# Optimization experiments

Measured on AMD Instinct MI355X. Metric: run time of the kernel, lower is better.

Reference implementation:

```python
import jax, jax.numpy as jnp
import numpy as np

IN, H, HC, HQ, OUT = 7, 64, 32, 16, 3  # input, shared hidden, cell hidden, head hidden, per-task out
B, S = 256, 2048


def setup_inputs() -> dict:
    key = jax.random.key(0)
    ks = iter(jax.random.split(key, 40))
    def p(shape, scale=0.1):
        return jax.random.normal(next(ks), shape, dtype=jnp.float32) * scale
    d = {}
    d['x'] = jax.random.normal(next(ks), (B, S, IN), dtype=jnp.float32)
    # shared LSTM (torch gate order i,f,g,o)
    d['W_ih_s'] = p((4 * H, IN)); d['W_hh_s'] = p((4 * H, H))
    d['b_ih_s'] = p((4 * H,));    d['b_hh_s'] = p((4 * H,))
    # attitude cell: input = [shared_h(64), x(7)]
    d['W_ih_a'] = p((4 * HC, H + IN)); d['W_hh_a'] = p((4 * HC, HC))
    d['b_ih_a'] = p((4 * HC,));        d['b_hh_a'] = p((4 * HC,))
    # velocity cell: input = [shared_h(64), delta_att(3), x(7)]
    d['W_ih_v'] = p((4 * HC, H + OUT + IN)); d['W_hh_v'] = p((4 * HC, HC))
    d['b_ih_v'] = p((4 * HC,));              d['b_hh_v'] = p((4 * HC,))
    # position cell: input = [shared_h(64), delta_vel(3)]
    d['W_ih_p'] = p((4 * HC, H + OUT)); d['W_hh_p'] = p((4 * HC, HC))
    d['b_ih_p'] = p((4 * HC,));         d['b_hh_p'] = p((4 * HC,))
    # per-task readout MLPs (dropout is identity in eval mode)
    d['Wa1'] = p((HQ, HC)); d['ba1'] = p((HQ,)); d['Wa2'] = p((OUT, HQ)); d['ba2'] = p((OUT,))
    d['Wv1'] = p((HQ, HC)); d['bv1'] = p((HQ,)); d['Wv2'] = p((OUT, HQ)); d['bv2'] = p((OUT,))
    d['Wp1'] = p((HQ, HC)); d['bp1'] = p((HQ,)); d['Wp2'] = p((OUT, HQ)); d['bp2'] = p((OUT,))
    return d


def lstm_cell(x, h, c, Wih, Whh, bih, bhh):
    z = x @ Wih.T + h @ Whh.T + bih + bhh
    i, f, g, o = jnp.split(z, 4, axis=-1)
    c = jax.nn.sigmoid(f) * c + jax.nn.sigmoid(i) * jnp.tanh(g)
    h = jax.nn.sigmoid(o) * jnp.tanh(c)
    return h, c


def mlp(h, W1, b1, W2, b2):
    return jax.nn.relu(h @ W1.T + b1) @ W2.T + b2


def reference(x, W_ih_s, W_hh_s, b_ih_s, b_hh_s,
              W_ih_a, W_hh_a, b_ih_a, b_hh_a,
              W_ih_v, W_hh_v, b_ih_v, b_hh_v,
              W_ih_p, W_hh_p, b_ih_p, b_hh_p,
              Wa1, ba1, Wa2, ba2, Wv1, bv1, Wv2, bv2, Wp1, bp1, Wp2, bp2):
    b = x.shape[0]
    z = lambda n: jnp.zeros((b, n), x.dtype)
    carry0 = (z(H), z(H), z(HC), z(HC), z(HC), z(HC), z(HC), z(HC))

    def step(carry, xt):
        hs, cs, ha, ca, hv, cv, hp, cp = carry
        hs, cs = lstm_cell(xt, hs, cs, W_ih_s, W_hh_s, b_ih_s, b_hh_s)
        ha, ca = lstm_cell(jnp.concatenate([hs, xt], -1), ha, ca,
                           W_ih_a, W_hh_a, b_ih_a, b_hh_a)
        d_att = mlp(ha, Wa1, ba1, Wa2, ba2)
        hv, cv = lstm_cell(jnp.concatenate([hs, jax.lax.stop_gradient(d_att), xt], -1),
                           hv, cv, W_ih_v, W_hh_v, b_ih_v, b_hh_v)
        d_vel = mlp(hv, Wv1, bv1, Wv2, bv2)
        hp, cp = lstm_cell(jnp.concatenate([hs, jax.lax.stop_gradient(d_vel)], -1),
                           hp, cp, W_ih_p, W_hh_p, b_ih_p, b_hh_p)
        d_pos = mlp(hp, Wp1, bp1, Wp2, bp2)
        out = jnp.concatenate([d_att, d_vel, d_pos], -1)  # [B, 9]
        return (hs, cs, ha, ca, hv, cv, hp, cp), out

    _, ys = jax.lax.scan(step, carry0, jnp.swapaxes(x, 0, 1))  # [S, B, 9]
    return jnp.swapaxes(ys, 0, 1)  # [B, S, 9]
```

## Files before the change

kernel.cpp:

```cpp
#include <hip/hip_runtime.h>

typedef unsigned int u32;

#define NIN 7
#define NB 256
#define NS 2048

__device__ __forceinline__ float fastrcp(float x){ return __builtin_amdgcn_rcpf(x); }
__device__ __forceinline__ float sigf(float x){ return fastrcp(1.f + __expf(-x)); }
__device__ __forceinline__ float tanhf_(float x){ return 1.f - 2.f*fastrcp(1.f + __expf(2.f*x)); }

__device__ __forceinline__ u32 pkh(float a, float b){
  unsigned short ua = __builtin_bit_cast(unsigned short, (_Float16)a);
  unsigned short ub = __builtin_bit_cast(unsigned short, (_Float16)b);
  return (u32)ua | ((u32)ub << 16);
}

template<int J>
__device__ __forceinline__ float rlf(float v){
  return __uint_as_float((unsigned)__builtin_amdgcn_readlane((int)__float_as_uint(v), J));
}
__device__ __forceinline__ float rlfv(float v, int j){
  return __uint_as_float((unsigned)__builtin_amdgcn_readlane((int)__float_as_uint(v), j));
}

__device__ __forceinline__ float mxl(float acc, u32 wp, float a){
  asm("v_fma_mix_f32 %0, %1, %2, %3 op_sel_hi:[1,0,0]"
      : "=v"(acc) : "v"(wp), "s"(a), "0"(acc));
  return acc;
}
__device__ __forceinline__ float mxh(float acc, u32 wp, float a){
  asm("v_fma_mix_f32 %0, %1, %2, %3 op_sel:[1,0,0] op_sel_hi:[1,0,0]"
      : "=v"(acc) : "v"(wp), "s"(a), "0"(acc));
  return acc;
}
__device__ __forceinline__ float mxlv(float acc, u32 wp, float a){
  asm("v_fma_mix_f32 %0, %1, %2, %3 op_sel_hi:[1,0,0]"
      : "=v"(acc) : "v"(wp), "v"(a), "0"(acc));
  return acc;
}
__device__ __forceinline__ float mxhv(float acc, u32 wp, float a){
  asm("v_fma_mix_f32 %0, %1, %2, %3 op_sel:[1,0,0] op_sel_hi:[1,0,0]"
      : "=v"(acc) : "v"(wp), "v"(a), "0"(acc));
  return acc;
}

__device__ __forceinline__ float gate4(float zi, float zf, float zg, float zo, float& c){
  c = sigf(zf)*c + sigf(zi)*tanhf_(zg);
  return sigf(zo)*tanhf_(c);
}

#define XD(a0, a1, KB, v0, v1) { \
  a0 = mxlv(a0, w[(KB)+0], (v0).x); a1 = mxhv(a1, w[(KB)+0], (v0).y); \
  a0 = mxlv(a0, w[(KB)+1], (v0).z); a1 = mxhv(a1, w[(KB)+1], (v0).w); \
  a0 = mxlv(a0, w[(KB)+2], (v1).x); a1 = mxhv(a1, w[(KB)+2], (v1).y); \
  a0 = mxlv(a0, w[(KB)+3], (v1).z); a1 = mxhv(a1, w[(KB)+3], (v1).w); }

#define MX2(a0, a1, s0, s1, KA, KS, SRC) { _Pragma("unroll") \
  for (int k_ = 0; k_ < 32; k_++){ \
    float e0_ = rlfv(SRC, 2*k_), e1_ = rlfv(SRC, 2*k_+1); \
    a0 = mxl(a0, w[(KA)+k_], e0_); a1 = mxh(a1, w[(KA)+k_], e1_); \
    s0 = mxl(s0, w[(KS)+k_], e0_); s1 = mxh(s1, w[(KS)+k_], e1_); } }

#define MX1(a0, a1, KA, SRC) { _Pragma("unroll") \
  for (int k_ = 0; k_ < 32; k_++){ \
    float e0_ = rlfv(SRC, 2*k_), e1_ = rlfv(SRC, 2*k_+1); \
    a0 = mxl(a0, w[(KA)+k_], e0_); a1 = mxh(a1, w[(KA)+k_], e1_); } }

#define MXH16(z0, z1, KB, SRC) { _Pragma("unroll") \
  for (int k_ = 0; k_ < 16; k_++){ \
    float e0_ = rlfv(SRC, 2*k_), e1_ = rlfv(SRC, 2*k_+1); \
    z0 = mxl(z0, w[(KB)+k_], e0_); z1 = mxh(z1, w[(KB)+k_], e1_); } }

#define MLPX(HS, M1B, B1V, M2B, B2V, dres) { \
  float q0_ = (B1V), q1_ = 0.f; \
  _Pragma("unroll") \
  for (int j_ = 0; j_ < 16; j_++){ \
    float e0_ = rlfv(HS, 2*j_), e1_ = rlfv(HS, 2*j_+1); \
    q0_ = mxl(q0_, w[(M1B)+j_], e0_); q1_ = mxh(q1_, w[(M1B)+j_], e1_); } \
  float qq_ = fmaxf(q0_+q1_, 0.f); \
  float f0_ = (B2V), f1_ = 0.f; \
  _Pragma("unroll") \
  for (int j_ = 0; j_ < 8; j_++){ \
    float e0_ = rlfv(qq_, 2*j_), e1_ = rlfv(qq_, 2*j_+1); \
    f0_ = mxl(f0_, w[(M2B)+j_], e0_); f1_ = mxh(f1_, w[(M2B)+j_], e1_); } \
  dres = f0_ + f1_; }

__global__ __launch_bounds__(512, 1) void mtinn_kernel(
    const float* __restrict__ x,
    const float* wihs, const float* whhs, const float* bihs, const float* bhhs,
    const float* wiha, const float* whha, const float* biha, const float* bhha,
    const float* wihv, const float* whhv, const float* bihv, const float* bhhv,
    const float* wihp, const float* whhp, const float* bihp, const float* bhhp,
    const float* wa1, const float* ba1, const float* wa2, const float* ba2,
    const float* wv1, const float* bv1, const float* wv2, const float* bv2,
    const float* wp1, const float* bp1, const float* wp2, const float* bp2,
    float* __restrict__ out)
{
  __shared__ __align__(16) float ZS[2][256];
  __shared__ __align__(16) float ZC[2][3][128];
  __shared__ __align__(16) float ZP[64];
  __shared__ __align__(16) float XL[4][8];

  const int tid  = threadIdx.x;
  const int wave = tid >> 6, lane = tid & 63, l = lane & 31;
  const int b    = blockIdx.x;
  const float* xb = x + (size_t)b * NS * NIN;

  const bool isWin = (wave != 0 && wave != 4);
  const bool isSh  = (wave==1 || wave==2 || wave==5 || wave==7);
  const int  qoff  = (wave==1) ? 0 : (wave==2) ? 64 : (wave==5) ? 128 : 192;
  const bool isTop = (wave >= 1 && wave <= 6);
  const int  tc    = (wave==1||wave==4) ? 0 : (wave==2||wave==5) ? 1 : 2;
  const int  trb   = (wave >= 4) ? 0 : 64;
  const int  wc    = (wave==1||wave==7) ? 0 : (wave==2||wave==5) ? 1 : 2;
  const int  wrb   = (wave <= 3) ? 64 : 0;

  u32 w[88];
#pragma unroll
  for (int i = 0; i < 88; i++) w[i] = 0u;
  float b1a=0.f,b1v=0.f,b1p=0.f,b2a=0.f,b2v=0.f,b2p=0.f;

  if (isWin){
    const float* wih = (wc==0) ? wiha : (wc==1) ? wihv : wihp;
    const float* bi  = (wc==0) ? biha : (wc==1) ? bihv : bihp;
    const float* bh  = (wc==0) ? bhha : (wc==1) ? bhhv : bhhp;
    const int L = (wc==0) ? 71 : (wc==1) ? 74 : 67;
    const int r = wrb + lane;
#pragma unroll
    for (int k=0;k<32;k++) w[16+k] = pkh(wih[r*L+2*k], wih[r*L+2*k+1]);
    const float bsum = bi[r] + bh[r];
    if (wc==0){
      w[48]=pkh(wih[r*L+64],wih[r*L+65]); w[49]=pkh(wih[r*L+66],wih[r*L+67]);
      w[50]=pkh(wih[r*L+68],wih[r*L+69]); w[51]=pkh(wih[r*L+70], bsum);
    } else if (wc==1){
      w[48]=pkh(wih[r*L+67],wih[r*L+68]); w[49]=pkh(wih[r*L+69],wih[r*L+70]);
      w[50]=pkh(wih[r*L+71],wih[r*L+72]); w[51]=pkh(wih[r*L+73], bsum);
    } else {
      w[51]=pkh(0.f, bsum);
    }
  }
  if (isTop){
    const float* whh = (tc==0) ? whha : (tc==1) ? whhv : whhp;
    const int r = trb + lane;
#pragma unroll
    for (int k=0;k<16;k++) w[k] = pkh(whh[r*32+2*k], whh[r*32+2*k+1]);
  }
  if (isSh){
    const int r = qoff + lane;
#pragma unroll
    for (int k=0;k<32;k++) w[52+k] = pkh(whhs[r*64+2*k], whhs[r*64+2*k+1]);
    w[84]=pkh(wihs[r*7+0],wihs[r*7+1]); w[85]=pkh(wihs[r*7+2],wihs[r*7+3]);
    w[86]=pkh(wihs[r*7+4],wihs[r*7+5]); w[87]=pkh(wihs[r*7+6], bihs[r]+bhhs[r]);
  }
  if (wave == 0){
    const int mi = lane & 15, mm = lane % 3;
#pragma unroll
    for (int k=0;k<16;k++){
      w[k]    = pkh(wa1[mi*32+2*k], wa1[mi*32+2*k+1]);
      w[16+k] = pkh(wv1[mi*32+2*k], wv1[mi*32+2*k+1]);
      w[32+k] = pkh(wp1[mi*32+2*k], wp1[mi*32+2*k+1]);
    }
#pragma unroll
    for (int k=0;k<8;k++){
      w[48+k] = pkh(wa2[mm*16+2*k], wa2[mm*16+2*k+1]);
      w[56+k] = pkh(wv2[mm*16+2*k], wv2[mm*16+2*k+1]);
      w[64+k] = pkh(wp2[mm*16+2*k], wp2[mm*16+2*k+1]);
    }
#pragma unroll
    for (int g=0; g<4; g++){
      int rr = g*32 + l;
      w[72+2*g]   = pkh(wihv[rr*74+64], wihv[rr*74+65]);
      w[72+2*g+1] = pkh(wihv[rr*74+66], 0.f);
      w[80+2*g]   = pkh(wihp[rr*67+64], wihp[rr*67+65]);
      w[80+2*g+1] = pkh(wihp[rr*67+66], 0.f);
    }
    b1a=ba1[mi]; b1v=bv1[mi]; b1p=bp1[mi];
    b2a=ba2[mm]; b2v=bv2[mm]; b2p=bp2[mm];
  }

  if (tid < 8){
    XL[0][tid] = (tid<7) ? xb[tid]         : 1.f;
    XL[1][tid] = (tid<7) ? xb[NIN+tid]     : 1.f;
    XL[2][tid] = (tid<7) ? xb[2*NIN+tid]   : 1.f;
    XL[3][tid] = 1.f;
  }
  if (tid < 384){
    int cell = tid >> 7, r = tid & 127;
    ZC[1][cell][r] = ((r >> 5) & 1) ? -40.f : 0.f;
  }
  __syncthreads();

  if (isSh){
    const float4* X0 = (const float4*)XL[0];
    float4 xa = X0[0], xb4 = X0[1];
    float s0=0.f, s1=0.f; XD(s0,s1,84,xa,xb4);
    ZS[0][qoff + lane] = s0 + s1;
  }
  __syncthreads();

  float c_s = 0.f, crep = 0.f;
  float c_a = 0.f, c_v = 0.f, c_p = 0.f;
  float zpart = 0.f;

  if (isWin){
    float zi_=ZS[0][lane], zf_=ZS[0][64+lane], zg_=ZS[0][128+lane], zo_=ZS[0][192+lane];
    float hsv = gate4(zi_,zf_,zg_,zo_, c_s);
    const float4* X0 = (const float4*)XL[0];
    float4 xa = X0[0], xb4 = X0[1];
    float a0=0.f, a1=0.f; XD(a0,a1,48,xa,xb4);
    if (isSh){
      const float4* X1 = (const float4*)XL[1];
      float4 xc = X1[0], xd = X1[1];
      float s0=0.f, s1=0.f; XD(s0,s1,84,xc,xd);
      MX2(a0,a1,s0,s1,16,52,hsv);
      ZS[1][qoff + lane] = s0 + s1;
    } else {
      MX1(a0,a1,16,hsv);
    }
    zpart = a0 + a1;
    if (wave == 7) ZP[lane] = zpart;
  }
  __syncthreads();

#pragma unroll 1
  for (int t = 0; t < NS; t++){
    float xpre = 0.f;
    if (wave == 0){
      if (lane < 7){
        const int tf = (t+3 < NS) ? t+3 : NS-1;
        xpre = xb[(size_t)tf*NIN + lane];
      }
    } else if (isTop){
      const float* zc = ZC[(t^1)&1][tc];
      float zi_=zc[l], zf_=zc[32+l], zg_=zc[64+l], zo_=zc[96+l];
      float h = gate4(zi_,zf_,zg_,zo_, crep);
      float z0 = (wave == 4) ? ZP[lane] : zpart;
      float z1 = 0.f;
      MXH16(z0,z1,0,h);
      ZC[t&1][tc][trb + lane] = z0 + z1;
    }
    __syncthreads();

    if (wave == 0){
      __builtin_amdgcn_s_setprio(1);
      const float* zca = ZC[t&1][0];
      const float* zcv = ZC[t&1][1];
      const float* zcp = ZC[t&1][2];
      float zai=zca[l], zaf=zca[32+l], zag=zca[64+l], zao=zca[96+l];
      float zvi=zcv[l], zvf=zcv[32+l], zvg=zcv[64+l], zvo=zcv[96+l];
      float zpi=zcp[l], zpf=zcp[32+l], zpg=zcp[64+l], zpo=zcp[96+l];
      float* ob = out + ((size_t)b*NS + t)*9;
      float ha = gate4(zai,zaf,zag,zao, c_a);
      float dA; MLPX(ha, 0, b1a, 48, b2a, dA);
      if (lane < 3) ob[lane] = dA;
      float dx=rlf<0>(dA), dy=rlf<1>(dA), dz=rlf<2>(dA);
      zvi = mxl(zvi, w[72], dx); zvi = mxh(zvi, w[72], dy); zvi = mxl(zvi, w[73], dz);
      zvf = mxl(zvf, w[74], dx); zvf = mxh(zvf, w[74], dy); zvf = mxl(zvf, w[75], dz);
      zvg = mxl(zvg, w[76], dx); zvg = mxh(zvg, w[76], dy); zvg = mxl(zvg, w[77], dz);
      zvo = mxl(zvo, w[78], dx); zvo = mxh(zvo, w[78], dy); zvo = mxl(zvo, w[79], dz);
      if (lane < 32){ float* zw = ZC[t&1][1]; zw[l]=zvi; zw[32+l]=zvf; zw[64+l]=zvg; zw[96+l]=zvo; }
      float hv = gate4(zvi,zvf,zvg,zvo, c_v);
      float dV; MLPX(hv, 16, b1v, 56, b2v, dV);
      if (lane < 3) ob[3+lane] = dV;
      dx=rlf<0>(dV); dy=rlf<1>(dV); dz=rlf<2>(dV);
      zpi = mxl(zpi, w[80], dx); zpi = mxh(zpi, w[80], dy); zpi = mxl(zpi, w[81], dz);
      zpf = mxl(zpf, w[82], dx); zpf = mxh(zpf, w[82], dy); zpf = mxl(zpf, w[83], dz);
      zpg = mxl(zpg, w[84], dx); zpg = mxh(zpg, w[84], dy); zpg = mxl(zpg, w[85], dz);
      zpo = mxl(zpo, w[86], dx); zpo = mxh(zpo, w[86], dy); zpo = mxl(zpo, w[87], dz);
      if (lane < 32){ float* zw = ZC[t&1][2]; zw[l]=zpi; zw[32+l]=zpf; zw[64+l]=zpg; zw[96+l]=zpo; }
      float hp_ = gate4(zpi,zpf,zpg,zpo, c_p);
      float dP; MLPX(hp_, 32, b1p, 64, b2p, dP);
      if (lane < 3) ob[6+lane] = dP;
      __builtin_amdgcn_s_setprio(0);
      if (lane < 7) XL[(t+3)&3][lane] = xpre;
    } else if (isWin){
      const float* Zsrc = ZS[(t+1)&1];
      float zi_=Zsrc[lane], zf_=Zsrc[64+lane], zg_=Zsrc[128+lane], zo_=Zsrc[192+lane];
      float hsv = gate4(zi_,zf_,zg_,zo_, c_s);
      const float4* X1 = (const float4*)XL[(t+1)&3];
      float4 xa = X1[0], xb4 = X1[1];
      float a0=0.f, a1=0.f; XD(a0,a1,48,xa,xb4);
      if (isSh){
        const float4* X2 = (const float4*)XL[(t+2)&3];
        float4 xc = X2[0], xd = X2[1];
        float s0=0.f, s1=0.f; XD(s0,s1,84,xc,xd);
        MX2(a0,a1,s0,s1,16,52,hsv);
        ZS[t&1][qoff + lane] = s0 + s1;
      } else {
        MX1(a0,a1,16,hsv);
      }
      zpart = a0 + a1;
      if (wave == 7) ZP[lane] = zpart;
    }
    __syncthreads();
  }
}

extern "C" void kernel_launch(void* const* d_in, const int* in_sizes, int n_in,
                              void* d_out, int out_size, void* d_ws, size_t ws_size,
                              hipStream_t stream) {
  (void)in_sizes; (void)n_in; (void)d_ws; (void)ws_size; (void)out_size;
  const float* X    = (const float*)d_in[0];
  const float* Wihs = (const float*)d_in[1];
  const float* Whhs = (const float*)d_in[2];
  const float* Bihs = (const float*)d_in[3];
  const float* Bhhs = (const float*)d_in[4];
  const float* Wiha = (const float*)d_in[5];
  const float* Whha = (const float*)d_in[6];
  const float* Biha = (const float*)d_in[7];
  const float* Bhha = (const float*)d_in[8];
  const float* Wihv = (const float*)d_in[9];
  const float* Whhv = (const float*)d_in[10];
  const float* Bihv = (const float*)d_in[11];
  const float* Bhhv = (const float*)d_in[12];
  const float* Wihp = (const float*)d_in[13];
  const float* Whhp = (const float*)d_in[14];
  const float* Bihp = (const float*)d_in[15];
  const float* Bhhp = (const float*)d_in[16];
  const float* Wa1  = (const float*)d_in[17];
  const float* Ba1  = (const float*)d_in[18];
  const float* Wa2  = (const float*)d_in[19];
  const float* Ba2  = (const float*)d_in[20];
  const float* Wv1  = (const float*)d_in[21];
  const float* Bv1  = (const float*)d_in[22];
  const float* Wv2  = (const float*)d_in[23];
  const float* Bv2  = (const float*)d_in[24];
  const float* Wp1  = (const float*)d_in[25];
  const float* Bp1  = (const float*)d_in[26];
  const float* Wp2  = (const float*)d_in[27];
  const float* Bp2  = (const float*)d_in[28];
  float* OUTP = (float*)d_out;

  mtinn_kernel<<<dim3(NB), dim3(512), 0, stream>>>(
      X, Wihs, Whhs, Bihs, Bhhs,
      Wiha, Whha, Biha, Bhha,
      Wihv, Whhv, Bihv, Bhhv,
      Wihp, Whhp, Bihp, Bhhp,
      Wa1, Ba1, Wa2, Ba2, Wv1, Bv1, Wv2, Bv2, Wp1, Bp1, Wp2, Bp2,
      OUTP);
}
```

Measured before the change: 3.178 ms.

## Move position MLP off critical wave and pass cell h via shared memory

The position-head MLP moves from wave 0 to wave 4, which computes it one step late from a double-buffered hp stored in shared memory. This shortens the serial chain that wave 0 runs each timestep. Wave 0 now publishes ha/hv/hp to shared memory instead of recomputing gates, so the recurrent-weight matvecs run on the input-weight waves and the ZC double buffer and the ZP handoff go away. The shared-LSTM gate evaluation is done once by wave 7 and broadcast through HS, rather than recomputed redundantly by every wave. The tradeoff is extra LDS traffic and a final epilogue step for the last timestep.

```diff
diff --git a/kernel.cpp b/kernel.cpp
--- a/kernel.cpp
+++ b/kernel.cpp
@@ -72,11 +72,11 @@
     float e0_ = rlfv(SRC, 2*k_), e1_ = rlfv(SRC, 2*k_+1); \
     z0 = mxl(z0, w[(KB)+k_], e0_); z1 = mxh(z1, w[(KB)+k_], e1_); } }
 
-#define MLPX(HS, M1B, B1V, M2B, B2V, dres) { \
+#define MLPX(HS_, M1B, B1V, M2B, B2V, dres) { \
   float q0_ = (B1V), q1_ = 0.f; \
   _Pragma("unroll") \
   for (int j_ = 0; j_ < 16; j_++){ \
-    float e0_ = rlfv(HS, 2*j_), e1_ = rlfv(HS, 2*j_+1); \
+    float e0_ = rlfv(HS_, 2*j_), e1_ = rlfv(HS_, 2*j_+1); \
     q0_ = mxl(q0_, w[(M1B)+j_], e0_); q1_ = mxh(q1_, w[(M1B)+j_], e1_); } \
   float qq_ = fmaxf(q0_+q1_, 0.f); \
   float f0_ = (B2V), f1_ = 0.f; \
@@ -98,8 +98,10 @@
     float* __restrict__ out)
 {
   __shared__ __align__(16) float ZS[2][256];
-  __shared__ __align__(16) float ZC[2][3][128];
-  __shared__ __align__(16) float ZP[64];
+  __shared__ __align__(16) float ZC[3][128];
+  __shared__ __align__(16) float HS[64];
+  __shared__ __align__(16) float HA[32], HV[32];
+  __shared__ __align__(16) float HPb[2][32];
   __shared__ __align__(16) float XL[4][8];
 
   const int tid  = threadIdx.x;
@@ -108,25 +110,26 @@
   const float* xb = x + (size_t)b * NS * NIN;
 
   const bool isWin = (wave != 0 && wave != 4);
-  const bool isSh  = (wave==1 || wave==2 || wave==5 || wave==7);
-  const int  qoff  = (wave==1) ? 0 : (wave==2) ? 64 : (wave==5) ? 128 : 192;
-  const bool isTop = (wave >= 1 && wave <= 6);
-  const int  tc    = (wave==1||wave==4) ? 0 : (wave==2||wave==5) ? 1 : 2;
-  const int  trb   = (wave >= 4) ? 0 : 64;
   const int  wc    = (wave==1||wave==7) ? 0 : (wave==2||wave==5) ? 1 : 2;
   const int  wrb   = (wave <= 3) ? 64 : 0;
+  const bool isSh  = (wave==1 || wave==2 || wave==6 || wave==7);
+  const int  qoff  = (wave==1) ? 0 : (wave==2) ? 64 : (wave==6) ? 128 : 192;
+  const int  mi = lane & 15, mm = lane % 3;
 
   u32 w[88];
 #pragma unroll
   for (int i = 0; i < 88; i++) w[i] = 0u;
-  float b1a=0.f,b1v=0.f,b1p=0.f,b2a=0.f,b2v=0.f,b2p=0.f;
+  float b1a=0.f,b2a=0.f,b1v=0.f,b2v=0.f,b1p=0.f,b2p=0.f;
 
   if (isWin){
     const float* wih = (wc==0) ? wiha : (wc==1) ? wihv : wihp;
+    const float* whh = (wc==0) ? whha : (wc==1) ? whhv : whhp;
     const float* bi  = (wc==0) ? biha : (wc==1) ? bihv : bihp;
     const float* bh  = (wc==0) ? bhha : (wc==1) ? bhhv : bhhp;
     const int L = (wc==0) ? 71 : (wc==1) ? 74 : 67;
     const int r = wrb + lane;
+#pragma unroll
+    for (int k=0;k<16;k++) w[k] = pkh(whh[r*32+2*k], whh[r*32+2*k+1]);
 #pragma unroll
     for (int k=0;k<32;k++) w[16+k] = pkh(wih[r*L+2*k], wih[r*L+2*k+1]);
     const float bsum = bi[r] + bh[r];
@@ -140,12 +143,6 @@
       w[51]=pkh(0.f, bsum);
     }
   }
-  if (isTop){
-    const float* whh = (tc==0) ? whha : (tc==1) ? whhv : whhp;
-    const int r = trb + lane;
-#pragma unroll
-    for (int k=0;k<16;k++) w[k] = pkh(whh[r*32+2*k], whh[r*32+2*k+1]);
-  }
   if (isSh){
     const int r = qoff + lane;
 #pragma unroll
@@ -154,18 +151,15 @@
     w[86]=pkh(wihs[r*7+4],wihs[r*7+5]); w[87]=pkh(wihs[r*7+6], bihs[r]+bhhs[r]);
   }
   if (wave == 0){
-    const int mi = lane & 15, mm = lane % 3;
 #pragma unroll
     for (int k=0;k<16;k++){
       w[k]    = pkh(wa1[mi*32+2*k], wa1[mi*32+2*k+1]);
       w[16+k] = pkh(wv1[mi*32+2*k], wv1[mi*32+2*k+1]);
-      w[32+k] = pkh(wp1[mi*32+2*k], wp1[mi*32+2*k+1]);
     }
 #pragma unroll
     for (int k=0;k<8;k++){
       w[48+k] = pkh(wa2[mm*16+2*k], wa2[mm*16+2*k+1]);
       w[56+k] = pkh(wv2[mm*16+2*k], wv2[mm*16+2*k+1]);
-      w[64+k] = pkh(wp2[mm*16+2*k], wp2[mm*16+2*k+1]);
     }
 #pragma unroll
     for (int g=0; g<4; g++){
@@ -175,20 +169,26 @@
       w[80+2*g]   = pkh(wihp[rr*67+64], wihp[rr*67+65]);
       w[80+2*g+1] = pkh(wihp[rr*67+66], 0.f);
     }
-    b1a=ba1[mi]; b1v=bv1[mi]; b1p=bp1[mi];
-    b2a=ba2[mm]; b2v=bv2[mm]; b2p=bp2[mm];
-  }
-
+    b1a=ba1[mi]; b2a=ba2[mm]; b1v=bv1[mi]; b2v=bv2[mm];
+  }
+  if (wave == 4){
+#pragma unroll
+    for (int k=0;k<16;k++) w[k] = pkh(wp1[mi*32+2*k], wp1[mi*32+2*k+1]);
+#pragma unroll
+    for (int k=0;k<8;k++)  w[16+k] = pkh(wp2[mm*16+2*k], wp2[mm*16+2*k+1]);
+    b1p=bp1[mi]; b2p=bp2[mm];
+  }
+
+  if (tid < 32) HA[tid]=0.f;
+  else if (tid < 64)  HV[tid-32]=0.f;
+  else if (tid < 96)  HPb[0][tid-64]=0.f;
+  else if (tid < 128) HPb[1][tid-96]=0.f;
   if (tid < 8){
     XL[0][tid] = (tid<7) ? xb[tid]         : 1.f;
     XL[1][tid] = (tid<7) ? xb[NIN+tid]     : 1.f;
     XL[2][tid] = (tid<7) ? xb[2*NIN+tid]   : 1.f;
     XL[3][tid] = 1.f;
   }
-  if (tid < 384){
-    int cell = tid >> 7, r = tid & 127;
-    ZC[1][cell][r] = ((r >> 5) & 1) ? -40.f : 0.f;
-  }
   __syncthreads();
 
   if (isSh){
@@ -199,7 +199,7 @@
   }
   __syncthreads();
 
-  float c_s = 0.f, crep = 0.f;
+  float c_s = 0.f;
   float c_a = 0.f, c_v = 0.f, c_p = 0.f;
   float zpart = 0.f;
 
@@ -219,7 +219,6 @@
       MX1(a0,a1,16,hsv);
     }
     zpart = a0 + a1;
-    if (wave == 7) ZP[lane] = zpart;
   }
   __syncthreads();
 
@@ -231,27 +230,35 @@
         const int tf = (t+3 < NS) ? t+3 : NS-1;
         xpre = xb[(size_t)tf*NIN + lane];
       }
-    } else if (isTop){
-      const float* zc = ZC[(t^1)&1][tc];
-      float zi_=zc[l], zf_=zc[32+l], zg_=zc[64+l], zo_=zc[96+l];
-      float h = gate4(zi_,zf_,zg_,zo_, crep);
-      float z0 = (wave == 4) ? ZP[lane] : zpart;
-      float z1 = 0.f;
+    } else if (wave == 4){
+      if (t > 0){
+        float hp_ = HPb[(t^1)&1][l];
+        float dP; MLPX(hp_, 0, b1p, 16, b2p, dP);
+        if (lane < 3) out[((size_t)b*NS + (t-1))*9 + 6 + lane] = dP;
+      }
+    } else {
+      const float* Hsrc = (wc==0) ? HA : (wc==1) ? HV : HPb[(t^1)&1];
+      float h = Hsrc[l];
+      if (wave == 7){
+        const float* Zsrc = ZS[(t+1)&1];
+        float zi_=Zsrc[lane], zf_=Zsrc[64+lane], zg_=Zsrc[128+lane], zo_=Zsrc[192+lane];
+        float hsv2 = gate4(zi_,zf_,zg_,zo_, c_s);
+        HS[lane] = hsv2;
+      }
+      float z0 = zpart, z1 = 0.f;
       MXH16(z0,z1,0,h);
-      ZC[t&1][tc][trb + lane] = z0 + z1;
+      ZC[wc][wrb + lane] = z0 + z1;
     }
     __syncthreads();
 
     if (wave == 0){
       __builtin_amdgcn_s_setprio(1);
-      const float* zca = ZC[t&1][0];
-      const float* zcv = ZC[t&1][1];
-      const float* zcp = ZC[t&1][2];
-      float zai=zca[l], zaf=zca[32+l], zag=zca[64+l], zao=zca[96+l];
-      float zvi=zcv[l], zvf=zcv[32+l], zvg=zcv[64+l], zvo=zcv[96+l];
-      float zpi=zcp[l], zpf=zcp[32+l], zpg=zcp[64+l], zpo=zcp[96+l];
+      float zai=ZC[0][l], zaf=ZC[0][32+l], zag=ZC[0][64+l], zao=ZC[0][96+l];
+      float zvi=ZC[1][l], zvf=ZC[1][32+l], zvg=ZC[1][64+l], zvo=ZC[1][96+l];
+      float zpi=ZC[2][l], zpf=ZC[2][32+l], zpg=ZC[2][64+l], zpo=ZC[2][96+l];
       float* ob = out + ((size_t)b*NS + t)*9;
       float ha = gate4(zai,zaf,zag,zao, c_a);
+      if (lane < 32) HA[lane] = ha;
       float dA; MLPX(ha, 0, b1a, 48, b2a, dA);
       if (lane < 3) ob[lane] = dA;
       float dx=rlf<0>(dA), dy=rlf<1>(dA), dz=rlf<2>(dA);
@@ -259,8 +266,8 @@
       zvf = mxl(zvf, w[74], dx); zvf = mxh(zvf, w[74], dy); zvf = mxl(zvf, w[75], dz);
       zvg = mxl(zvg, w[76], dx); zvg = mxh(zvg, w[76], dy); zvg = mxl(zvg, w[77], dz);
       zvo = mxl(zvo, w[78], dx); zvo = mxh(zvo, w[78], dy); zvo = mxl(zvo, w[79], dz);
-      if (lane < 32){ float* zw = ZC[t&1][1]; zw[l]=zvi; zw[32+l]=zvf; zw[64+l]=zvg; zw[96+l]=zvo; }
       float hv = gate4(zvi,zvf,zvg,zvo, c_v);
+      if (lane < 32) HV[lane] = hv;
       float dV; MLPX(hv, 16, b1v, 56, b2v, dV);
       if (lane < 3) ob[3+lane] = dV;
       dx=rlf<0>(dV); dy=rlf<1>(dV); dz=rlf<2>(dV);
@@ -268,16 +275,12 @@
       zpf = mxl(zpf, w[82], dx); zpf = mxh(zpf, w[82], dy); zpf = mxl(zpf, w[83], dz);
       zpg = mxl(zpg, w[84], dx); zpg = mxh(zpg, w[84], dy); zpg = mxl(zpg, w[85], dz);
       zpo = mxl(zpo, w[86], dx); zpo = mxh(zpo, w[86], dy); zpo = mxl(zpo, w[87], dz);
-      if (lane < 32){ float* zw = ZC[t&1][2]; zw[l]=zpi; zw[32+l]=zpf; zw[64+l]=zpg; zw[96+l]=zpo; }
       float hp_ = gate4(zpi,zpf,zpg,zpo, c_p);
-      float dP; MLPX(hp_, 32, b1p, 64, b2p, dP);
-      if (lane < 3) ob[6+lane] = dP;
+      if (lane < 32) HPb[t&1][lane] = hp_;
       __builtin_amdgcn_s_setprio(0);
       if (lane < 7) XL[(t+3)&3][lane] = xpre;
     } else if (isWin){
-      const float* Zsrc = ZS[(t+1)&1];
-      float zi_=Zsrc[lane], zf_=Zsrc[64+lane], zg_=Zsrc[128+lane], zo_=Zsrc[192+lane];
-      float hsv = gate4(zi_,zf_,zg_,zo_, c_s);
+      float hsv = HS[lane];
       const float4* X1 = (const float4*)XL[(t+1)&3];
       float4 xa = X1[0], xb4 = X1[1];
       float a0=0.f, a1=0.f; XD(a0,a1,48,xa,xb4);
@@ -291,9 +294,14 @@
         MX1(a0,a1,16,hsv);
       }
       zpart = a0 + a1;
-      if (wave == 7) ZP[lane] = zpart;
     }
     __syncthreads();
+  }
+
+  if (wave == 4){
+    float hp_ = HPb[(NS-1)&1][l];
+    float dP; MLPX(hp_, 0, b1p, 16, b2p, dP);
+    if (lane < 3) out[((size_t)b*NS + (NS-1))*9 + 6 + lane] = dP;
   }
 }
 
```

Result: faster. 2.871 ms (-9.7%).
